# Performance work log

Hardware: AMD Instinct MI355X
Metric: run time of the kernel (lower is better)

The kernel has to match this reference:

```python
import jax, jax.numpy as jnp
import numpy as np

OUT, N_GROUPS, GROUP = 11008, 32, 128
IN = N_GROUPS * GROUP  # 4096
TOKENS = 2048


def setup_inputs() -> dict:
    key = jax.random.key(0)
    k_x, k_w, k_sc, k_s, k_b = jax.random.split(key, 5)
    x = jax.random.normal(k_x, (TOKENS, IN), dtype=jnp.float32)
    # quantized 4-bit signed weights in [-7, 7] (stored int8 in torch; int32 here)
    w_q = jax.random.randint(k_w, (OUT, N_GROUPS, GROUP), -7, 8, dtype=jnp.int32)
    # per-(out, group) positive scales, bounded away from zero like the clamp(min=1e-5)
    scales = jax.random.uniform(k_sc, (OUT, N_GROUPS, 1), dtype=jnp.float32, minval=1e-3, maxval=0.05)
    # smoothing vector: positive, bounded away from zero (it divides x)
    s = jax.random.uniform(k_s, (IN,), dtype=jnp.float32, minval=0.5, maxval=2.0)
    bias = jax.random.normal(k_b, (OUT,), dtype=jnp.float32)
    return {"x": x, "w_q": w_q, "scales": scales, "s": s, "bias": bias}


def reference(x, w_q, scales, s, bias):
    orig_dtype = x.dtype
    # group-wise dequant: [O, G, K] * [O, G, 1] -> [O, I]
    w_recon = (w_q.astype(jnp.float32) * scales).reshape(OUT, IN)
    x_f = x.astype(jnp.float32) / s  # smoothing-scale division
    y = x_f @ w_recon.T + bias
    return y.astype(orig_dtype)
```

## Files before the change

### kernel.cpp

```cpp
#include <hip/hip_runtime.h>
#include <hip/hip_bf16.h>

#define TOKENS  2048
#define IN_DIM  4096
#define OUT_DIM 11008
#define NGROUPS 32

#define BM 128
#define BN 128
#define BKB 128
#define THREADS 512
#define NKT   (IN_DIM / BKB)
#define BUFB  32768
#define BOFF  16384

using f32x4  = __attribute__((ext_vector_type(4))) float;
using i32x4  = __attribute__((ext_vector_type(4))) int;
using bf16x8 = __attribute__((ext_vector_type(8))) short;

typedef __attribute__((address_space(3))) char as3c;

static __device__ __forceinline__ short f2bf(float f) {
    union { float f; unsigned u; } v; v.f = f;
    unsigned r = v.u + 0x7FFFu + ((v.u >> 16) & 1u);
    return (short)(r >> 16);
}

static __device__ __forceinline__ int pack4(int a, int b, int c, int d) {
    return (a & 255) | ((b & 255) << 8) | ((c & 255) << 16) | ((d & 255) << 24);
}

#define SB0 __builtin_amdgcn_sched_barrier(0)
#define LDSR(dst, addr)   asm volatile("ds_read_b128 %0, %1" : "=v"(dst) : "v"(addr))
#define WAITL(n) do { asm volatile("s_waitcnt lgkmcnt(" #n ")"); SB0; } while (0)
#define WAITV(n) do { asm volatile("s_waitcnt vmcnt(" #n ")");  SB0; } while (0)

__global__ __launch_bounds__(256) void prep_a_kernel(
    const float* __restrict__ x, const float* __restrict__ s,
    char* __restrict__ Aq, float* __restrict__ sx)
{
    const int row = blockIdx.x, t = threadIdx.x;
    const float* xp = x + (size_t)row * IN_DIM + t * 16;
    const float* sp = s + t * 16;
    f32x4 v[4];
    float m = 0.f;
    #pragma unroll
    for (int q = 0; q < 4; ++q) {
        f32x4 xv = *(const f32x4*)(xp + q * 4);
        f32x4 sv = *(const f32x4*)(sp + q * 4);
        #pragma unroll
        for (int e = 0; e < 4; ++e) {
            v[q][e] = xv[e] / sv[e];
            m = fmaxf(m, fabsf(v[q][e]));
        }
    }
    #pragma unroll
    for (int off = 32; off; off >>= 1) m = fmaxf(m, __shfl_xor(m, off));
    __shared__ float wm[4];
    if ((t & 63) == 0) wm[t >> 6] = m;
    __syncthreads();
    m = fmaxf(fmaxf(wm[0], wm[1]), fmaxf(wm[2], wm[3]));
    m = fmaxf(m, 1e-20f);
    const float inv = 127.0f / m;
    i32x4 pk;
    #pragma unroll
    for (int q = 0; q < 4; ++q)
        pk[q] = pack4((int)rintf(v[q][0] * inv), (int)rintf(v[q][1] * inv),
                      (int)rintf(v[q][2] * inv), (int)rintf(v[q][3] * inv));
    ((i32x4*)(Aq + (size_t)row * IN_DIM))[t] = pk;
    if (t == 0) sx[row] = m * (1.0f / 127.0f);
}

__global__ __launch_bounds__(256) void prep_b_kernel(
    const int* __restrict__ wq, char* __restrict__ Bq)
{
    const int idx = blockIdx.x * 256 + threadIdx.x;
    const int* wp = wq + (size_t)idx * 16;
    i32x4 w0 = *(const i32x4*)wp, w1 = *(const i32x4*)(wp + 4);
    i32x4 w2 = *(const i32x4*)(wp + 8), w3 = *(const i32x4*)(wp + 12);
    i32x4 pk;
    pk[0] = pack4(w0[0], w0[1], w0[2], w0[3]);
    pk[1] = pack4(w1[0], w1[1], w1[2], w1[3]);
    pk[2] = pack4(w2[0], w2[1], w2[2], w2[3]);
    pk[3] = pack4(w3[0], w3[1], w3[2], w3[3]);
    ((i32x4*)Bq)[idx] = pk;
}

__global__ __launch_bounds__(256) void prep_sc_kernel(
    const float* __restrict__ scales, float* __restrict__ scT)
{
    const int idx = blockIdx.x * 256 + threadIdx.x;
    const int g = idx / OUT_DIM;
    const int o = idx - g * OUT_DIM;
    scT[idx] = scales[o * NGROUPS + g];
}

__global__ __launch_bounds__(THREADS, 4) void awq_gemm_i8(
    const char* __restrict__ Aq, const char* __restrict__ Bq,
    const float* __restrict__ scT, const float* __restrict__ sx,
    const float* __restrict__ bias, float* __restrict__ out)
{
    const int rb = blockIdx.x;
    const int bm = (rb >> 3) & 15;
    const int bn = (((rb >> 3) >> 4) << 3) + (rb & 7);
    if (bn >= OUT_DIM / BN) return;

    __shared__ char smem[2 * BUFB];
    as3c* ldsb = (as3c*)smem;
    const unsigned lbase = (unsigned)(size_t)ldsb;

    const int tid  = threadIdx.x;
    const int lane = tid & 63;
    const int w    = tid >> 6;
    const int wr   = w >> 2;
    const int wc   = w & 3;
    const int fr   = lane & 15;
    const int fko  = lane >> 4;

    const int h7 = fr & 7;
    const unsigned swz0 = (unsigned)(((0 * 4 + fko) ^ h7) * 16);
    const unsigned swz1 = (unsigned)(((1 * 4 + fko) ^ h7) * 16);
    const unsigned aB0 = lbase + (wr * 64 + fr) * 128 + swz0;
    const unsigned aB1 = lbase + (wr * 64 + fr) * 128 + swz1;
    const unsigned bB0 = lbase + BOFF + (wc * 32 + fr) * 128 + swz0;
    const unsigned bB1 = lbase + BOFF + (wc * 32 + fr) * 128 + swz1;

    const int srow = tid >> 3;
    const int sg   = ((tid & 7) ^ (srow & 7)) * 16;
    const char* aSrc = Aq + (size_t)(bm * BM + srow) * IN_DIM + sg;
    const char* bSrc = Bq + (size_t)(bn * BN + srow) * IN_DIM + sg;

    const float* scp = scT + bn * BN + wc * 32 + fr;

#define STG_A(Q, KT, P) __builtin_amdgcn_global_load_lds( \
    (const __attribute__((address_space(1))) void*)(const void*)(aSrc + (size_t)((Q) * 64) * IN_DIM + (KT) * BKB), \
    (__attribute__((address_space(3))) void*)(ldsb + (P) * BUFB + (Q) * 8192 + tid * 16), 16, 0, 0)
#define STG_B(Q, KT, P) __builtin_amdgcn_global_load_lds( \
    (const __attribute__((address_space(1))) void*)(const void*)(bSrc + (size_t)((Q) * 64) * IN_DIM + (KT) * BKB), \
    (__attribute__((address_space(3))) void*)(ldsb + (P) * BUFB + BOFF + (Q) * 8192 + tid * 16), 16, 0, 0)

#define SCV_GLOAD(D0, D1, G) do { \
    asm volatile("global_load_dword %0, %1, off" : "=v"(D0) : "v"(scp + (size_t)(G) * OUT_DIM)); \
    asm volatile("global_load_dword %0, %1, off" : "=v"(D1) : "v"(scp + (size_t)(G) * OUT_DIM + 16)); \
    SB0; } while (0)

    f32x4 accf[4][2];
    #pragma unroll
    for (int i = 0; i < 4; ++i) {
        accf[i][0] = (f32x4){0.f, 0.f, 0.f, 0.f};
        accf[i][1] = (f32x4){0.f, 0.f, 0.f, 0.f};
    }

    float c0, c1, n0 = 0.f, n1 = 0.f;

    STG_A(0, 0, 0); STG_A(1, 0, 0); STG_B(0, 0, 0); STG_B(1, 0, 0);
    SCV_GLOAD(c0, c1, 0);
    STG_A(0, 1, 1); STG_A(1, 1, 1); STG_B(0, 1, 1); STG_B(1, 1, 1);
    WAITV(4);
    __builtin_amdgcn_s_barrier();
    SB0;

    for (int t = 0; t < NKT; ++t) {
        const int P = t & 1;
        const unsigned po = (unsigned)(P * BUFB);
        const bool haveN = (t + 1 < NKT);
        const bool haveS = (t + 2 < NKT);

        i32x4 a[4][2], b[2][2];
        LDSR(b[0][0], bB0 + po);        LDSR(b[0][1], bB1 + po);
        LDSR(b[1][0], bB0 + po + 2048); LDSR(b[1][1], bB1 + po + 2048);
        #pragma unroll
        for (int i = 0; i < 4; ++i) {
            LDSR(a[i][0], aB0 + po + i * 2048);
            LDSR(a[i][1], aB1 + po + i * 2048);
        }
        WAITL(0);
        __builtin_amdgcn_s_barrier();
        SB0;

        if (haveN) SCV_GLOAD(n0, n1, t + 1);
        if (haveS) { STG_A(0, t + 2, P); STG_A(1, t + 2, P);
                     STG_B(0, t + 2, P); STG_B(1, t + 2, P); }

        __builtin_amdgcn_s_setprio(1);
        #pragma unroll
        for (int i = 0; i < 4; ++i) {
            i32x4 t0 = __builtin_amdgcn_mfma_i32_16x16x64_i8(a[i][0], b[0][0], (i32x4){0,0,0,0}, 0, 0, 0);
            t0       = __builtin_amdgcn_mfma_i32_16x16x64_i8(a[i][1], b[0][1], t0, 0, 0, 0);
            i32x4 t1 = __builtin_amdgcn_mfma_i32_16x16x64_i8(a[i][0], b[1][0], (i32x4){0,0,0,0}, 0, 0, 0);
            t1       = __builtin_amdgcn_mfma_i32_16x16x64_i8(a[i][1], b[1][1], t1, 0, 0, 0);
            #pragma unroll
            for (int e = 0; e < 4; ++e) {
                accf[i][0][e] += (float)t0[e] * c0;
                accf[i][1][e] += (float)t1[e] * c1;
            }
        }
        __builtin_amdgcn_s_setprio(0);

        if (t < NKT - 2) { WAITV(4); } else { WAITV(0); }
        __builtin_amdgcn_s_barrier();
        SB0;
        if (haveN) { c0 = n0; c1 = n1; }
    }

    #pragma unroll
    for (int i = 0; i < 4; ++i) {
        const int row = bm * BM + wr * 64 + i * 16 + fko * 4;
        const f32x4 sxv = *(const f32x4*)(sx + row);
        #pragma unroll
        for (int j = 0; j < 2; ++j) {
            const int col = bn * BN + wc * 32 + j * 16 + fr;
            const float bv = bias[col];
            #pragma unroll
            for (int e = 0; e < 4; ++e)
                out[(size_t)(row + e) * OUT_DIM + col] = accf[i][j][e] * sxv[e] + bv;
        }
    }

#undef STG_A
#undef STG_B
#undef SCV_GLOAD
}

__global__ __launch_bounds__(256) void awq_gemm_fb(
    const float* __restrict__ x, const int* __restrict__ wq,
    const float* __restrict__ scales, const float* __restrict__ s,
    const float* __restrict__ bias, float* __restrict__ out)
{
    __shared__ short As[128][32];
    __shared__ short Bs[128][32];
    const int tid = threadIdx.x, lane = tid & 63, wave = tid >> 6;
    const int nbn = OUT_DIM / 128;
    const int bm = blockIdx.x / nbn, bn = blockIdx.x % nbn;
    const int srow = tid >> 1, scol = (tid & 1) * 16;
    const int wm = (wave >> 1) * 64, wn = (wave & 1) * 64;
    f32x4 acc[4][4];
    #pragma unroll
    for (int i = 0; i < 4; ++i)
        #pragma unroll
        for (int j = 0; j < 4; ++j) acc[i][j] = (f32x4){0.f, 0.f, 0.f, 0.f};
    const float* xrow = x + (size_t)(bm * 128 + srow) * IN_DIM;
    const int* wrow = wq + (size_t)(bn * 128 + srow) * IN_DIM;
    const float* scrow = scales + (size_t)(bn * 128 + srow) * NGROUPS;
    const int fr = lane & 15, fk = (lane >> 4) * 8, fq = lane >> 4;
    for (int kt = 0; kt < IN_DIM / 32; ++kt) {
        const int k0 = kt * 32;
        {
            const float* xp = xrow + k0 + scol;
            const float* sp = s + k0 + scol;
            short tmp[16];
            #pragma unroll
            for (int q = 0; q < 4; ++q) {
                f32x4 xv = *(const f32x4*)(xp + q * 4);
                f32x4 sv = *(const f32x4*)(sp + q * 4);
                #pragma unroll
                for (int e = 0; e < 4; ++e) tmp[q * 4 + e] = f2bf(xv[e] / sv[e]);
            }
            #pragma unroll
            for (int e = 0; e < 16; ++e) As[srow][scol + e] = tmp[e];
        }
        {
            const float sc = scrow[kt >> 2];
            const int* wp = wrow + k0 + scol;
            short tmp[16];
            #pragma unroll
            for (int q = 0; q < 4; ++q) {
                i32x4 wv = *(const i32x4*)(wp + q * 4);
                #pragma unroll
                for (int e = 0; e < 4; ++e) tmp[q * 4 + e] = f2bf((float)wv[e] * sc);
            }
            #pragma unroll
            for (int e = 0; e < 16; ++e) Bs[srow][scol + e] = tmp[e];
        }
        __syncthreads();
        bf16x8 a[4], b[4];
        #pragma unroll
        for (int i = 0; i < 4; ++i) a[i] = *(const bf16x8*)&As[wm + i * 16 + fr][fk];
        #pragma unroll
        for (int j = 0; j < 4; ++j) b[j] = *(const bf16x8*)&Bs[wn + j * 16 + fr][fk];
        #pragma unroll
        for (int i = 0; i < 4; ++i)
            #pragma unroll
            for (int j = 0; j < 4; ++j)
                acc[i][j] = __builtin_amdgcn_mfma_f32_16x16x32_bf16(a[i], b[j], acc[i][j], 0, 0, 0);
        __syncthreads();
    }
    #pragma unroll
    for (int i = 0; i < 4; ++i) {
        const int row = bm * 128 + wm + i * 16 + fq * 4;
        #pragma unroll
        for (int j = 0; j < 4; ++j) {
            const int col = bn * 128 + wn + j * 16 + fr;
            const float bv = bias[col];
            #pragma unroll
            for (int e = 0; e < 4; ++e)
                out[(size_t)(row + e) * OUT_DIM + col] = acc[i][j][e] + bv;
        }
    }
}

extern "C" void kernel_launch(void* const* d_in, const int* in_sizes, int n_in,
                              void* d_out, int out_size, void* d_ws, size_t ws_size,
                              hipStream_t stream) {
    const float* x      = (const float*)d_in[0];
    const int*   wq     = (const int*)  d_in[1];
    const float* scales = (const float*)d_in[2];
    const float* s      = (const float*)d_in[3];
    const float* bias   = (const float*)d_in[4];
    float* out = (float*)d_out;

    const size_t off_sx = (size_t)TOKENS * IN_DIM;
    const size_t off_bq = off_sx + 8192;
    const size_t off_sc = off_bq + (size_t)OUT_DIM * IN_DIM;
    const size_t need   = off_sc + (size_t)OUT_DIM * NGROUPS * 4;

    if (ws_size >= need) {
        char*  Aq  = (char*)d_ws;
        float* sxw = (float*)((char*)d_ws + off_sx);
        char*  Bq  = (char*)d_ws + off_bq;
        float* scT = (float*)((char*)d_ws + off_sc);
        prep_a_kernel<<<TOKENS, 256, 0, stream>>>(x, s, Aq, sxw);
        prep_b_kernel<<<OUT_DIM * IN_DIM / 16 / 256, 256, 0, stream>>>(wq, Bq);
        prep_sc_kernel<<<OUT_DIM * NGROUPS / 256, 256, 0, stream>>>(scales, scT);
        awq_gemm_i8<<<1408, THREADS, 0, stream>>>(Aq, Bq, scT, sxw, bias, out);
    } else {
        awq_gemm_fb<<<(TOKENS / 128) * (OUT_DIM / 128), 256, 0, stream>>>(x, wq, scales, s, bias, out);
    }
}
```

Before: 179.6 us.

## Switch int8 GEMM to 32x32x32 MFMA with 4 waves and deferred scaling

Rewrites the main int8 GEMM to use 256 threads (4 waves, each owning a 64x64 sub-tile) with 32x32x32 int8 MFMA instructions in place of 16x16x64. LDS reads are interleaved with MFMAs through staged lgkmcnt waits. The per-group float rescale of the integer partials is deferred into the next iteration so it overlaps the next tile's MFMAs. The aim is fewer instructions and more register reuse per wave, at the cost of larger accumulator register use and lower occupancy (launch bound changed to 2 blocks per CU).

```diff
diff --git a/kernel.cpp b/kernel.cpp
--- a/kernel.cpp
+++ b/kernel.cpp
@@ -9,13 +9,14 @@
 #define BM 128
 #define BN 128
 #define BKB 128
-#define THREADS 512
+#define THREADS 256
 #define NKT   (IN_DIM / BKB)
 #define BUFB  32768
 #define BOFF  16384
 
 using f32x4  = __attribute__((ext_vector_type(4))) float;
 using i32x4  = __attribute__((ext_vector_type(4))) int;
+using i32x16 = __attribute__((ext_vector_type(16))) int;
 using bf16x8 = __attribute__((ext_vector_type(8))) short;
 
 typedef __attribute__((address_space(3))) char as3c;
@@ -31,7 +32,7 @@
 }
 
 #define SB0 __builtin_amdgcn_sched_barrier(0)
-#define LDSR(dst, addr)   asm volatile("ds_read_b128 %0, %1" : "=v"(dst) : "v"(addr))
+#define LDSRO(dst, addr, off) asm volatile("ds_read_b128 %0, %1 offset:" #off : "=v"(dst) : "v"(addr))
 #define WAITL(n) do { asm volatile("s_waitcnt lgkmcnt(" #n ")"); SB0; } while (0)
 #define WAITV(n) do { asm volatile("s_waitcnt vmcnt(" #n ")");  SB0; } while (0)
 
@@ -95,7 +96,7 @@
     scT[idx] = scales[o * NGROUPS + g];
 }
 
-__global__ __launch_bounds__(THREADS, 4) void awq_gemm_i8(
+__global__ __launch_bounds__(THREADS, 2) void awq_gemm_i8(
     const char* __restrict__ Aq, const char* __restrict__ Bq,
     const float* __restrict__ scT, const float* __restrict__ sx,
     const float* __restrict__ bias, float* __restrict__ out)
@@ -112,114 +113,160 @@
     const int tid  = threadIdx.x;
     const int lane = tid & 63;
     const int w    = tid >> 6;
-    const int wr   = w >> 2;
-    const int wc   = w & 3;
-    const int fr   = lane & 15;
-    const int fko  = lane >> 4;
-
-    const int h7 = fr & 7;
-    const unsigned swz0 = (unsigned)(((0 * 4 + fko) ^ h7) * 16);
-    const unsigned swz1 = (unsigned)(((1 * 4 + fko) ^ h7) * 16);
-    const unsigned aB0 = lbase + (wr * 64 + fr) * 128 + swz0;
-    const unsigned aB1 = lbase + (wr * 64 + fr) * 128 + swz1;
-    const unsigned bB0 = lbase + BOFF + (wc * 32 + fr) * 128 + swz0;
-    const unsigned bB1 = lbase + BOFF + (wc * 32 + fr) * 128 + swz1;
+    const int wr   = w >> 1;
+    const int wc   = w & 1;
+    const int lr   = lane & 31;
+    const int hi   = lane >> 5;
+    const int h7   = lr & 7;
+
+    const unsigned aRow = lbase + (unsigned)((wr * 64 + lr) * 128);
+    const unsigned bRow = lbase + BOFF + (unsigned)((wc * 64 + lr) * 128);
+    const unsigned aS0 = aRow + (unsigned)(((0 + hi) ^ h7) * 16);
+    const unsigned aS1 = aRow + (unsigned)(((2 + hi) ^ h7) * 16);
+    const unsigned aS2 = aRow + (unsigned)(((4 + hi) ^ h7) * 16);
+    const unsigned aS3 = aRow + (unsigned)(((6 + hi) ^ h7) * 16);
+    const unsigned bS0 = bRow + (unsigned)(((0 + hi) ^ h7) * 16);
+    const unsigned bS1 = bRow + (unsigned)(((2 + hi) ^ h7) * 16);
+    const unsigned bS2 = bRow + (unsigned)(((4 + hi) ^ h7) * 16);
+    const unsigned bS3 = bRow + (unsigned)(((6 + hi) ^ h7) * 16);
 
     const int srow = tid >> 3;
     const int sg   = ((tid & 7) ^ (srow & 7)) * 16;
     const char* aSrc = Aq + (size_t)(bm * BM + srow) * IN_DIM + sg;
     const char* bSrc = Bq + (size_t)(bn * BN + srow) * IN_DIM + sg;
 
-    const float* scp = scT + bn * BN + wc * 32 + fr;
-
-#define STG_A(Q, KT, P) __builtin_amdgcn_global_load_lds( \
-    (const __attribute__((address_space(1))) void*)(const void*)(aSrc + (size_t)((Q) * 64) * IN_DIM + (KT) * BKB), \
-    (__attribute__((address_space(3))) void*)(ldsb + (P) * BUFB + (Q) * 8192 + tid * 16), 16, 0, 0)
-#define STG_B(Q, KT, P) __builtin_amdgcn_global_load_lds( \
-    (const __attribute__((address_space(1))) void*)(const void*)(bSrc + (size_t)((Q) * 64) * IN_DIM + (KT) * BKB), \
-    (__attribute__((address_space(3))) void*)(ldsb + (P) * BUFB + BOFF + (Q) * 8192 + tid * 16), 16, 0, 0)
-
-#define SCV_GLOAD(D0, D1, G) do { \
-    asm volatile("global_load_dword %0, %1, off" : "=v"(D0) : "v"(scp + (size_t)(G) * OUT_DIM)); \
-    asm volatile("global_load_dword %0, %1, off" : "=v"(D1) : "v"(scp + (size_t)(G) * OUT_DIM + 16)); \
+    const float* scp = scT + bn * BN + wc * 64 + lr;
+
+#define STG_A(Q, SRC, P) __builtin_amdgcn_global_load_lds( \
+    (const __attribute__((address_space(1))) void*)(const void*)((SRC) + (size_t)((Q) * 32) * IN_DIM), \
+    (__attribute__((address_space(3))) void*)(ldsb + (P) * BUFB + (Q) * 4096 + tid * 16), 16, 0, 0)
+#define STG_B(Q, SRC, P) __builtin_amdgcn_global_load_lds( \
+    (const __attribute__((address_space(1))) void*)(const void*)((SRC) + (size_t)((Q) * 32) * IN_DIM), \
+    (__attribute__((address_space(3))) void*)(ldsb + (P) * BUFB + BOFF + (Q) * 4096 + tid * 16), 16, 0, 0)
+
+#define SCV(D0, D1, PTR) do { \
+    asm volatile("global_load_dword %0, %1, off" : "=v"(D0) : "v"(PTR)); \
+    asm volatile("global_load_dword %0, %1, off" : "=v"(D1) : "v"((PTR) + 32)); \
     SB0; } while (0)
 
-    f32x4 accf[4][2];
-    #pragma unroll
-    for (int i = 0; i < 4; ++i) {
-        accf[i][0] = (f32x4){0.f, 0.f, 0.f, 0.f};
-        accf[i][1] = (f32x4){0.f, 0.f, 0.f, 0.f};
-    }
-
-    float c0, c1, n0 = 0.f, n1 = 0.f;
-
-    STG_A(0, 0, 0); STG_A(1, 0, 0); STG_B(0, 0, 0); STG_B(1, 0, 0);
-    SCV_GLOAD(c0, c1, 0);
-    STG_A(0, 1, 1); STG_A(1, 1, 1); STG_B(0, 1, 1); STG_B(1, 1, 1);
-    WAITV(4);
+    float accf[2][2][16];
+    #pragma unroll
+    for (int i = 0; i < 2; ++i)
+        #pragma unroll
+        for (int j = 0; j < 2; ++j)
+            #pragma unroll
+            for (int e = 0; e < 16; ++e) accf[i][j][e] = 0.f;
+
+    i32x16 acc[2][2];
+    const i32x16 Z = {0,0,0,0,0,0,0,0,0,0,0,0,0,0,0,0};
+
+    float c0, c1, n0 = 0.f, n1 = 0.f, p0 = 0.f, p1 = 0.f;
+
+    STG_A(0, aSrc, 0); STG_A(1, aSrc, 0); STG_A(2, aSrc, 0); STG_A(3, aSrc, 0);
+    STG_B(0, bSrc, 0); STG_B(1, bSrc, 0); STG_B(2, bSrc, 0); STG_B(3, bSrc, 0);
+    SCV(c0, c1, scp);
+    STG_A(0, aSrc + BKB, 1); STG_A(1, aSrc + BKB, 1); STG_A(2, aSrc + BKB, 1); STG_A(3, aSrc + BKB, 1);
+    STG_B(0, bSrc + BKB, 1); STG_B(1, bSrc + BKB, 1); STG_B(2, bSrc + BKB, 1); STG_B(3, bSrc + BKB, 1);
+    WAITV(8);
     __builtin_amdgcn_s_barrier();
     SB0;
 
+    const char* aStg = aSrc + 2 * BKB;
+    const char* bStg = bSrc + 2 * BKB;
+    const float* scN = scp + OUT_DIM;
+
     for (int t = 0; t < NKT; ++t) {
-        const int P = t & 1;
-        const unsigned po = (unsigned)(P * BUFB);
-        const bool haveN = (t + 1 < NKT);
-        const bool haveS = (t + 2 < NKT);
-
-        i32x4 a[4][2], b[2][2];
-        LDSR(b[0][0], bB0 + po);        LDSR(b[0][1], bB1 + po);
-        LDSR(b[1][0], bB0 + po + 2048); LDSR(b[1][1], bB1 + po + 2048);
-        #pragma unroll
-        for (int i = 0; i < 4; ++i) {
-            LDSR(a[i][0], aB0 + po + i * 2048);
-            LDSR(a[i][1], aB1 + po + i * 2048);
-        }
+        const unsigned po = (unsigned)((t & 1) * BUFB);
+        i32x4 a[2][4], b[2][4];
+        const unsigned pa0 = aS0 + po, pa1 = aS1 + po, pa2 = aS2 + po, pa3 = aS3 + po;
+        const unsigned pb0 = bS0 + po, pb1 = bS1 + po, pb2 = bS2 + po, pb3 = bS3 + po;
+        LDSRO(a[0][0], pa0, 0); LDSRO(a[1][0], pa0, 4096);
+        LDSRO(b[0][0], pb0, 0); LDSRO(b[1][0], pb0, 4096);
+        LDSRO(a[0][1], pa1, 0); LDSRO(a[1][1], pa1, 4096);
+        LDSRO(b[0][1], pb1, 0); LDSRO(b[1][1], pb1, 4096);
+        LDSRO(a[0][2], pa2, 0); LDSRO(a[1][2], pa2, 4096);
+        LDSRO(b[0][2], pb2, 0); LDSRO(b[1][2], pb2, 4096);
+        LDSRO(a[0][3], pa3, 0); LDSRO(a[1][3], pa3, 4096);
+        LDSRO(b[0][3], pb3, 0); LDSRO(b[1][3], pb3, 4096);
+
+        if (t > 0) {
+            #pragma unroll
+            for (int i = 0; i < 2; ++i)
+                #pragma unroll
+                for (int e = 0; e < 16; ++e) {
+                    accf[i][0][e] += (float)acc[i][0][e] * p0;
+                    accf[i][1][e] += (float)acc[i][1][e] * p1;
+                }
+        }
+
+        __builtin_amdgcn_s_setprio(1);
+        WAITL(12);
+        acc[0][0] = __builtin_amdgcn_mfma_i32_32x32x32_i8(a[0][0], b[0][0], Z, 0, 0, 0);
+        acc[0][1] = __builtin_amdgcn_mfma_i32_32x32x32_i8(a[0][0], b[1][0], Z, 0, 0, 0);
+        acc[1][0] = __builtin_amdgcn_mfma_i32_32x32x32_i8(a[1][0], b[0][0], Z, 0, 0, 0);
+        acc[1][1] = __builtin_amdgcn_mfma_i32_32x32x32_i8(a[1][0], b[1][0], Z, 0, 0, 0);
+        WAITL(8);
+        acc[0][0] = __builtin_amdgcn_mfma_i32_32x32x32_i8(a[0][1], b[0][1], acc[0][0], 0, 0, 0);
+        acc[0][1] = __builtin_amdgcn_mfma_i32_32x32x32_i8(a[0][1], b[1][1], acc[0][1], 0, 0, 0);
+        acc[1][0] = __builtin_amdgcn_mfma_i32_32x32x32_i8(a[1][1], b[0][1], acc[1][0], 0, 0, 0);
+        acc[1][1] = __builtin_amdgcn_mfma_i32_32x32x32_i8(a[1][1], b[1][1], acc[1][1], 0, 0, 0);
+        WAITL(4);
+        acc[0][0] = __builtin_amdgcn_mfma_i32_32x32x32_i8(a[0][2], b[0][2], acc[0][0], 0, 0, 0);
+        acc[0][1] = __builtin_amdgcn_mfma_i32_32x32x32_i8(a[0][2], b[1][2], acc[0][1], 0, 0, 0);
+        acc[1][0] = __builtin_amdgcn_mfma_i32_32x32x32_i8(a[1][2], b[0][2], acc[1][0], 0, 0, 0);
+        acc[1][1] = __builtin_amdgcn_mfma_i32_32x32x32_i8(a[1][2], b[1][2], acc[1][1], 0, 0, 0);
         WAITL(0);
         __builtin_amdgcn_s_barrier();
         SB0;
-
-        if (haveN) SCV_GLOAD(n0, n1, t + 1);
-        if (haveS) { STG_A(0, t + 2, P); STG_A(1, t + 2, P);
-                     STG_B(0, t + 2, P); STG_B(1, t + 2, P); }
-
-        __builtin_amdgcn_s_setprio(1);
-        #pragma unroll
-        for (int i = 0; i < 4; ++i) {
-            i32x4 t0 = __builtin_amdgcn_mfma_i32_16x16x64_i8(a[i][0], b[0][0], (i32x4){0,0,0,0}, 0, 0, 0);
-            t0       = __builtin_amdgcn_mfma_i32_16x16x64_i8(a[i][1], b[0][1], t0, 0, 0, 0);
-            i32x4 t1 = __builtin_amdgcn_mfma_i32_16x16x64_i8(a[i][0], b[1][0], (i32x4){0,0,0,0}, 0, 0, 0);
-            t1       = __builtin_amdgcn_mfma_i32_16x16x64_i8(a[i][1], b[1][1], t1, 0, 0, 0);
-            #pragma unroll
-            for (int e = 0; e < 4; ++e) {
-                accf[i][0][e] += (float)t0[e] * c0;
-                accf[i][1][e] += (float)t1[e] * c1;
-            }
-        }
+        acc[0][0] = __builtin_amdgcn_mfma_i32_32x32x32_i8(a[0][3], b[0][3], acc[0][0], 0, 0, 0);
+        acc[0][1] = __builtin_amdgcn_mfma_i32_32x32x32_i8(a[0][3], b[1][3], acc[0][1], 0, 0, 0);
+        acc[1][0] = __builtin_amdgcn_mfma_i32_32x32x32_i8(a[1][3], b[0][3], acc[1][0], 0, 0, 0);
+        acc[1][1] = __builtin_amdgcn_mfma_i32_32x32x32_i8(a[1][3], b[1][3], acc[1][1], 0, 0, 0);
         __builtin_amdgcn_s_setprio(0);
 
-        if (t < NKT - 2) { WAITV(4); } else { WAITV(0); }
+        const bool haveN = (t + 1 < NKT);
+        if (haveN) SCV(n0, n1, scN);
+        if (t + 2 < NKT) {
+            STG_A(0, aStg, (t & 1)); STG_A(1, aStg, (t & 1)); STG_A(2, aStg, (t & 1)); STG_A(3, aStg, (t & 1));
+            STG_B(0, bStg, (t & 1)); STG_B(1, bStg, (t & 1)); STG_B(2, bStg, (t & 1)); STG_B(3, bStg, (t & 1));
+        }
+        aStg += BKB; bStg += BKB; scN += OUT_DIM;
+
+        if (t < NKT - 2) { WAITV(8); } else { WAITV(0); }
         __builtin_amdgcn_s_barrier();
         SB0;
+        p0 = c0; p1 = c1;
         if (haveN) { c0 = n0; c1 = n1; }
     }
 
     #pragma unroll
-    for (int i = 0; i < 4; ++i) {
-        const int row = bm * BM + wr * 64 + i * 16 + fko * 4;
-        const f32x4 sxv = *(const f32x4*)(sx + row);
-        #pragma unroll
-        for (int j = 0; j < 2; ++j) {
-            const int col = bn * BN + wc * 32 + j * 16 + fr;
-            const float bv = bias[col];
-            #pragma unroll
-            for (int e = 0; e < 4; ++e)
-                out[(size_t)(row + e) * OUT_DIM + col] = accf[i][j][e] * sxv[e] + bv;
+    for (int i = 0; i < 2; ++i)
+        #pragma unroll
+        for (int e = 0; e < 16; ++e) {
+            accf[i][0][e] += (float)acc[i][0][e] * p0;
+            accf[i][1][e] += (float)acc[i][1][e] * p1;
+        }
+
+    const int colBase = bn * BN + wc * 64 + lr;
+    const float bv0 = bias[colBase];
+    const float bv1 = bias[colBase + 32];
+    #pragma unroll
+    for (int i = 0; i < 2; ++i) {
+        #pragma unroll
+        for (int q = 0; q < 4; ++q) {
+            const int r0 = bm * BM + wr * 64 + i * 32 + q * 8 + hi * 4;
+            const f32x4 sxv = *(const f32x4*)(sx + r0);
+            #pragma unroll
+            for (int e = 0; e < 4; ++e) {
+                out[(size_t)(r0 + e) * OUT_DIM + colBase]      = accf[i][0][q * 4 + e] * sxv[e] + bv0;
+                out[(size_t)(r0 + e) * OUT_DIM + colBase + 32] = accf[i][1][q * 4 + e] * sxv[e] + bv1;
+            }
         }
     }
 
 #undef STG_A
 #undef STG_B
-#undef SCV_GLOAD
+#undef SCV
 }
 
 __global__ __launch_bounds__(256) void awq_gemm_fb(
```

Measured after the change: 229.9 us. +28.0%, slower.

## Load weight fragments straight to registers and software-pipeline the k-loop

Applied to the files above, without the earlier changes.

Weight (B) tiles no longer go through LDS. Each wave loads its int8 MFMA fragments directly from global memory into registers, one k-step ahead, alongside the per-group scales. That halves the LDS footprint to just the activation buffers. The k-loop is unrolled by two, with fixed ping-pong buffers and immediate-offset ds_reads interleaved with the MFMAs, and the next activation stage is issued mid-iteration. This cuts LDS traffic and barrier-bound stalls, but waves that share columns now fetch the same B data twice from global/L2, and register pressure rises.

```diff
diff --git a/kernel.cpp b/kernel.cpp
--- a/kernel.cpp
+++ b/kernel.cpp
@@ -11,8 +11,7 @@
 #define BKB 128
 #define THREADS 512
 #define NKT   (IN_DIM / BKB)
-#define BUFB  32768
-#define BOFF  16384
+#define BUFB  16384
 
 using f32x4  = __attribute__((ext_vector_type(4))) float;
 using i32x4  = __attribute__((ext_vector_type(4))) int;
@@ -31,7 +30,7 @@
 }
 
 #define SB0 __builtin_amdgcn_sched_barrier(0)
-#define LDSR(dst, addr)   asm volatile("ds_read_b128 %0, %1" : "=v"(dst) : "v"(addr))
+#define LDSRO(dst, addr, off) asm volatile("ds_read_b128 %0, %1 offset:" #off : "=v"(dst) : "v"(addr))
 #define WAITL(n) do { asm volatile("s_waitcnt lgkmcnt(" #n ")"); SB0; } while (0)
 #define WAITV(n) do { asm volatile("s_waitcnt vmcnt(" #n ")");  SB0; } while (0)
 
@@ -122,27 +121,42 @@
     const unsigned swz1 = (unsigned)(((1 * 4 + fko) ^ h7) * 16);
     const unsigned aB0 = lbase + (wr * 64 + fr) * 128 + swz0;
     const unsigned aB1 = lbase + (wr * 64 + fr) * 128 + swz1;
-    const unsigned bB0 = lbase + BOFF + (wc * 32 + fr) * 128 + swz0;
-    const unsigned bB1 = lbase + BOFF + (wc * 32 + fr) * 128 + swz1;
 
     const int srow = tid >> 3;
     const int sg   = ((tid & 7) ^ (srow & 7)) * 16;
     const char* aSrc = Aq + (size_t)(bm * BM + srow) * IN_DIM + sg;
-    const char* bSrc = Bq + (size_t)(bn * BN + srow) * IN_DIM + sg;
 
     const float* scp = scT + bn * BN + wc * 32 + fr;
 
-#define STG_A(Q, KT, P) __builtin_amdgcn_global_load_lds( \
-    (const __attribute__((address_space(1))) void*)(const void*)(aSrc + (size_t)((Q) * 64) * IN_DIM + (KT) * BKB), \
+    const char* bfp0 = Bq + (size_t)(bn * BN + wc * 32 + fr) * IN_DIM + fko * 16;
+    const char* bfp1 = bfp0 + (size_t)16 * IN_DIM;
+
+#define STG_A(Q, OFFB, P) __builtin_amdgcn_global_load_lds( \
+    (const __attribute__((address_space(1))) void*)(const void*)(aStg + (OFFB) + (size_t)((Q) * 64) * IN_DIM), \
     (__attribute__((address_space(3))) void*)(ldsb + (P) * BUFB + (Q) * 8192 + tid * 16), 16, 0, 0)
-#define STG_B(Q, KT, P) __builtin_amdgcn_global_load_lds( \
-    (const __attribute__((address_space(1))) void*)(const void*)(bSrc + (size_t)((Q) * 64) * IN_DIM + (KT) * BKB), \
-    (__attribute__((address_space(3))) void*)(ldsb + (P) * BUFB + BOFF + (Q) * 8192 + tid * 16), 16, 0, 0)
-
-#define SCV_GLOAD(D0, D1, G) do { \
-    asm volatile("global_load_dword %0, %1, off" : "=v"(D0) : "v"(scp + (size_t)(G) * OUT_DIM)); \
-    asm volatile("global_load_dword %0, %1, off" : "=v"(D1) : "v"(scp + (size_t)(G) * OUT_DIM + 16)); \
+
+#define BFRAG4(D00, D01, D10, D11, O0, O1) do { \
+    asm volatile("global_load_dwordx4 %0, %1, off offset:" #O0 : "=v"(D00) : "v"(bfp0)); \
+    asm volatile("global_load_dwordx4 %0, %1, off offset:" #O1 : "=v"(D01) : "v"(bfp0)); \
+    asm volatile("global_load_dwordx4 %0, %1, off offset:" #O0 : "=v"(D10) : "v"(bfp1)); \
+    asm volatile("global_load_dwordx4 %0, %1, off offset:" #O1 : "=v"(D11) : "v"(bfp1)); \
     SB0; } while (0)
+
+#define SCV(D0, D1, PTR) do { \
+    asm volatile("global_load_dword %0, %1, off" : "=v"(D0) : "v"(PTR)); \
+    asm volatile("global_load_dword %0, %1, off" : "=v"(D1) : "v"((PTR) + 16)); \
+    SB0; } while (0)
+
+#define MMI(A0, A1, B00, B01, B10, B11, F0, F1) do { \
+    i32x4 t0 = __builtin_amdgcn_mfma_i32_16x16x64_i8(A0, B00, (i32x4){0,0,0,0}, 0, 0, 0); \
+    t0       = __builtin_amdgcn_mfma_i32_16x16x64_i8(A1, B01, t0, 0, 0, 0); \
+    i32x4 t1 = __builtin_amdgcn_mfma_i32_16x16x64_i8(A0, B10, (i32x4){0,0,0,0}, 0, 0, 0); \
+    t1       = __builtin_amdgcn_mfma_i32_16x16x64_i8(A1, B11, t1, 0, 0, 0); \
+    _Pragma("unroll") \
+    for (int e = 0; e < 4; ++e) { \
+        F0[e] += (float)t0[e] * c0; \
+        F1[e] += (float)t1[e] * c1; \
+    } } while (0)
 
     f32x4 accf[4][2];
     #pragma unroll
@@ -151,56 +165,78 @@
         accf[i][1] = (f32x4){0.f, 0.f, 0.f, 0.f};
     }
 
+    i32x4 b0_00, b0_01, b0_10, b0_11;
+    i32x4 b1_00, b1_01, b1_10, b1_11;
     float c0, c1, n0 = 0.f, n1 = 0.f;
 
-    STG_A(0, 0, 0); STG_A(1, 0, 0); STG_B(0, 0, 0); STG_B(1, 0, 0);
-    SCV_GLOAD(c0, c1, 0);
-    STG_A(0, 1, 1); STG_A(1, 1, 1); STG_B(0, 1, 1); STG_B(1, 1, 1);
-    WAITV(4);
+    const char*  aStg = aSrc;
+    const float* scN  = scp + OUT_DIM;
+
+    STG_A(0, 0, 0); STG_A(1, 0, 0);
+    SB0;
+    BFRAG4(b0_00, b0_01, b0_10, b0_11, 0, 64);
+    SCV(c0, c1, scp);
+    STG_A(0, 128, 1); STG_A(1, 128, 1);
+    SB0;
+    WAITV(2);
     __builtin_amdgcn_s_barrier();
     SB0;
 
-    for (int t = 0; t < NKT; ++t) {
-        const int P = t & 1;
-        const unsigned po = (unsigned)(P * BUFB);
-        const bool haveN = (t + 1 < NKT);
-        const bool haveS = (t + 2 < NKT);
-
-        i32x4 a[4][2], b[2][2];
-        LDSR(b[0][0], bB0 + po);        LDSR(b[0][1], bB1 + po);
-        LDSR(b[1][0], bB0 + po + 2048); LDSR(b[1][1], bB1 + po + 2048);
-        #pragma unroll
-        for (int i = 0; i < 4; ++i) {
-            LDSR(a[i][0], aB0 + po + i * 2048);
-            LDSR(a[i][1], aB1 + po + i * 2048);
-        }
+    for (int it = 0; it < NKT / 2; ++it) {
+        const bool last = (it == NKT / 2 - 1);
+        i32x4 a00, a01, a10, a11, a20, a21, a30, a31;
+
+        LDSRO(a00, aB0, 0);    LDSRO(a01, aB1, 0);
+        LDSRO(a10, aB0, 2048); LDSRO(a11, aB1, 2048);
+        BFRAG4(b1_00, b1_01, b1_10, b1_11, 128, 192);
+        SCV(n0, n1, scN);
+        __builtin_amdgcn_s_setprio(1);
+        WAITL(2);
+        LDSRO(a20, aB0, 4096); LDSRO(a21, aB1, 4096);
+        MMI(a00, a01, b0_00, b0_01, b0_10, b0_11, accf[0][0], accf[0][1]);
+        WAITL(2);
+        LDSRO(a30, aB0, 6144); LDSRO(a31, aB1, 6144);
+        MMI(a10, a11, b0_00, b0_01, b0_10, b0_11, accf[1][0], accf[1][1]);
+        WAITL(2);
+        MMI(a20, a21, b0_00, b0_01, b0_10, b0_11, accf[2][0], accf[2][1]);
         WAITL(0);
         __builtin_amdgcn_s_barrier();
         SB0;
-
-        if (haveN) SCV_GLOAD(n0, n1, t + 1);
-        if (haveS) { STG_A(0, t + 2, P); STG_A(1, t + 2, P);
-                     STG_B(0, t + 2, P); STG_B(1, t + 2, P); }
-
+        if (!last) { STG_A(0, 256, 0); STG_A(1, 256, 0); }
+        SB0;
+        MMI(a30, a31, b0_00, b0_01, b0_10, b0_11, accf[3][0], accf[3][1]);
+        __builtin_amdgcn_s_setprio(0);
+        if (!last) { WAITV(2); } else { WAITV(0); }
+        __builtin_amdgcn_s_barrier();
+        SB0;
+        c0 = n0; c1 = n1;
+
+        LDSRO(a00, aB0, 16384); LDSRO(a01, aB1, 16384);
+        LDSRO(a10, aB0, 18432); LDSRO(a11, aB1, 18432);
+        if (!last) { BFRAG4(b0_00, b0_01, b0_10, b0_11, 256, 320); SCV(n0, n1, scN + OUT_DIM); }
         __builtin_amdgcn_s_setprio(1);
-        #pragma unroll
-        for (int i = 0; i < 4; ++i) {
-            i32x4 t0 = __builtin_amdgcn_mfma_i32_16x16x64_i8(a[i][0], b[0][0], (i32x4){0,0,0,0}, 0, 0, 0);
-            t0       = __builtin_amdgcn_mfma_i32_16x16x64_i8(a[i][1], b[0][1], t0, 0, 0, 0);
-            i32x4 t1 = __builtin_amdgcn_mfma_i32_16x16x64_i8(a[i][0], b[1][0], (i32x4){0,0,0,0}, 0, 0, 0);
-            t1       = __builtin_amdgcn_mfma_i32_16x16x64_i8(a[i][1], b[1][1], t1, 0, 0, 0);
-            #pragma unroll
-            for (int e = 0; e < 4; ++e) {
-                accf[i][0][e] += (float)t0[e] * c0;
-                accf[i][1][e] += (float)t1[e] * c1;
-            }
-        }
+        WAITL(2);
+        LDSRO(a20, aB0, 20480); LDSRO(a21, aB1, 20480);
+        MMI(a00, a01, b1_00, b1_01, b1_10, b1_11, accf[0][0], accf[0][1]);
+        WAITL(2);
+        LDSRO(a30, aB0, 22528); LDSRO(a31, aB1, 22528);
+        MMI(a10, a11, b1_00, b1_01, b1_10, b1_11, accf[1][0], accf[1][1]);
+        WAITL(2);
+        MMI(a20, a21, b1_00, b1_01, b1_10, b1_11, accf[2][0], accf[2][1]);
+        WAITL(0);
+        __builtin_amdgcn_s_barrier();
+        SB0;
+        if (!last) { STG_A(0, 384, 1); STG_A(1, 384, 1); }
+        SB0;
+        MMI(a30, a31, b1_00, b1_01, b1_10, b1_11, accf[3][0], accf[3][1]);
         __builtin_amdgcn_s_setprio(0);
-
-        if (t < NKT - 2) { WAITV(4); } else { WAITV(0); }
+        if (!last) { WAITV(2); } else { WAITV(0); }
         __builtin_amdgcn_s_barrier();
         SB0;
-        if (haveN) { c0 = n0; c1 = n1; }
+        if (!last) { c0 = n0; c1 = n1; }
+
+        aStg += 256; scN += 2 * OUT_DIM;
+        bfp0 += 256; bfp1 += 256;
     }
 
     #pragma unroll
@@ -218,8 +254,9 @@
     }
 
 #undef STG_A
-#undef STG_B
-#undef SCV_GLOAD
+#undef BFRAG4
+#undef SCV
+#undef MMI
 }
 
 __global__ __launch_bounds__(256) void awq_gemm_fb(
```

Result: slower. 409.6 us (+128.1%).

## Widen int8 GEMM tile to 128x256 with BK=64 and a two-step unrolled pipeline

Applied to the files above, without the earlier changes.

Changes the int8 MFMA GEMM block tile from 128x128 with K-step 128 to 128x256 with K-step 64, so each wave now covers 64x64 outputs. The main loop is unrolled over the two LDS buffers, so LDS reads use fixed immediate offsets, and each group scale is loaded once per 128-wide group. The aim is more reuse of each staged A tile and fewer blocks (768 instead of 1408) loading overlapping data. In exchange it uses more accumulator registers, lowers the launch-bounds occupancy hint from 4 to 2, and makes the swizzle and the wait counts more intricate.

```diff
diff --git a/kernel.cpp b/kernel.cpp
--- a/kernel.cpp
+++ b/kernel.cpp
@@ -7,12 +7,13 @@
 #define NGROUPS 32
 
 #define BM 128
-#define BN 128
-#define BKB 128
+#define BN 256
+#define BK 64
 #define THREADS 512
-#define NKT   (IN_DIM / BKB)
-#define BUFB  32768
-#define BOFF  16384
+#define NT    (IN_DIM / BK)
+#define ABYTES (BM * BK)
+#define BBYTES (BN * BK)
+#define BUFB  (ABYTES + BBYTES)
 
 using f32x4  = __attribute__((ext_vector_type(4))) float;
 using i32x4  = __attribute__((ext_vector_type(4))) int;
@@ -31,7 +32,7 @@
 }
 
 #define SB0 __builtin_amdgcn_sched_barrier(0)
-#define LDSR(dst, addr)   asm volatile("ds_read_b128 %0, %1" : "=v"(dst) : "v"(addr))
+#define LDSRO(dst, addr, off) asm volatile("ds_read_b128 %0, %1 offset:" #off : "=v"(dst) : "v"(addr))
 #define WAITL(n) do { asm volatile("s_waitcnt lgkmcnt(" #n ")"); SB0; } while (0)
 #define WAITV(n) do { asm volatile("s_waitcnt vmcnt(" #n ")");  SB0; } while (0)
 
@@ -95,7 +96,7 @@
     scT[idx] = scales[o * NGROUPS + g];
 }
 
-__global__ __launch_bounds__(THREADS, 4) void awq_gemm_i8(
+__global__ __launch_bounds__(THREADS, 2) void awq_gemm_i8(
     const char* __restrict__ Aq, const char* __restrict__ Bq,
     const float* __restrict__ scT, const float* __restrict__ sx,
     const float* __restrict__ bias, float* __restrict__ out)
@@ -117,90 +118,110 @@
     const int fr   = lane & 15;
     const int fko  = lane >> 4;
 
-    const int h7 = fr & 7;
-    const unsigned swz0 = (unsigned)(((0 * 4 + fko) ^ h7) * 16);
-    const unsigned swz1 = (unsigned)(((1 * 4 + fko) ^ h7) * 16);
-    const unsigned aB0 = lbase + (wr * 64 + fr) * 128 + swz0;
-    const unsigned aB1 = lbase + (wr * 64 + fr) * 128 + swz1;
-    const unsigned bB0 = lbase + BOFF + (wc * 32 + fr) * 128 + swz0;
-    const unsigned bB1 = lbase + BOFF + (wc * 32 + fr) * 128 + swz1;
-
-    const int srow = tid >> 3;
-    const int sg   = ((tid & 7) ^ (srow & 7)) * 16;
-    const char* aSrc = Aq + (size_t)(bm * BM + srow) * IN_DIM + sg;
-    const char* bSrc = Bq + (size_t)(bn * BN + srow) * IN_DIM + sg;
-
-    const float* scp = scT + bn * BN + wc * 32 + fr;
-
-#define STG_A(Q, KT, P) __builtin_amdgcn_global_load_lds( \
-    (const __attribute__((address_space(1))) void*)(const void*)(aSrc + (size_t)((Q) * 64) * IN_DIM + (KT) * BKB), \
-    (__attribute__((address_space(3))) void*)(ldsb + (P) * BUFB + (Q) * 8192 + tid * 16), 16, 0, 0)
-#define STG_B(Q, KT, P) __builtin_amdgcn_global_load_lds( \
-    (const __attribute__((address_space(1))) void*)(const void*)(bSrc + (size_t)((Q) * 64) * IN_DIM + (KT) * BKB), \
-    (__attribute__((address_space(3))) void*)(ldsb + (P) * BUFB + BOFF + (Q) * 8192 + tid * 16), 16, 0, 0)
-
-#define SCV_GLOAD(D0, D1, G) do { \
-    asm volatile("global_load_dword %0, %1, off" : "=v"(D0) : "v"(scp + (size_t)(G) * OUT_DIM)); \
-    asm volatile("global_load_dword %0, %1, off" : "=v"(D1) : "v"(scp + (size_t)(G) * OUT_DIM + 16)); \
+    const unsigned sw4  = (unsigned)((fko ^ (fr & 3)) * 16);
+    const unsigned aAddr = lbase + (unsigned)((wr * 64 + fr) * 64) + sw4;
+    const unsigned bAddr = lbase + ABYTES + (unsigned)((wc * 64 + fr) * 64) + sw4;
+
+    const int sr = tid >> 2;
+    const int sg = ((tid & 3) ^ (sr & 3)) * 16;
+    const char* aSrc  = Aq + (size_t)(bm * BM + sr) * IN_DIM + sg;
+    const char* bSrc  = Bq + (size_t)(bn * BN + sr) * IN_DIM + sg;
+    const char* bSrc2 = bSrc + (size_t)128 * IN_DIM;
+
+    const float* scp = scT + bn * BN + wc * 64 + fr;
+
+#define STG(PA, PB, PB2, P) do { \
+    __builtin_amdgcn_global_load_lds((const __attribute__((address_space(1))) void*)(const void*)(PA), \
+        (__attribute__((address_space(3))) void*)(ldsb + (P) * BUFB + tid * 16), 16, 0, 0); \
+    __builtin_amdgcn_global_load_lds((const __attribute__((address_space(1))) void*)(const void*)(PB), \
+        (__attribute__((address_space(3))) void*)(ldsb + (P) * BUFB + ABYTES + tid * 16), 16, 0, 0); \
+    __builtin_amdgcn_global_load_lds((const __attribute__((address_space(1))) void*)(const void*)(PB2), \
+        (__attribute__((address_space(3))) void*)(ldsb + (P) * BUFB + ABYTES + 8192 + tid * 16), 16, 0, 0); \
     SB0; } while (0)
 
-    f32x4 accf[4][2];
-    #pragma unroll
-    for (int i = 0; i < 4; ++i) {
-        accf[i][0] = (f32x4){0.f, 0.f, 0.f, 0.f};
-        accf[i][1] = (f32x4){0.f, 0.f, 0.f, 0.f};
-    }
-
-    float c0, c1, n0 = 0.f, n1 = 0.f;
-
-    STG_A(0, 0, 0); STG_A(1, 0, 0); STG_B(0, 0, 0); STG_B(1, 0, 0);
-    SCV_GLOAD(c0, c1, 0);
-    STG_A(0, 1, 1); STG_A(1, 1, 1); STG_B(0, 1, 1); STG_B(1, 1, 1);
-    WAITV(4);
+#define SCV4(D0, D1, D2, D3, PTR) do { \
+    asm volatile("global_load_dword %0, %1, off"            : "=v"(D0) : "v"(PTR)); \
+    asm volatile("global_load_dword %0, %1, off offset:64"  : "=v"(D1) : "v"(PTR)); \
+    asm volatile("global_load_dword %0, %1, off offset:128" : "=v"(D2) : "v"(PTR)); \
+    asm volatile("global_load_dword %0, %1, off offset:192" : "=v"(D3) : "v"(PTR)); \
+    SB0; } while (0)
+
+#define QUADJ(J, CJ) do { \
+    i32x4 t0 = __builtin_amdgcn_mfma_i32_16x16x64_i8(a[0], b[J], (i32x4){0,0,0,0}, 0, 0, 0); \
+    i32x4 t1 = __builtin_amdgcn_mfma_i32_16x16x64_i8(a[1], b[J], (i32x4){0,0,0,0}, 0, 0, 0); \
+    i32x4 t2 = __builtin_amdgcn_mfma_i32_16x16x64_i8(a[2], b[J], (i32x4){0,0,0,0}, 0, 0, 0); \
+    i32x4 t3 = __builtin_amdgcn_mfma_i32_16x16x64_i8(a[3], b[J], (i32x4){0,0,0,0}, 0, 0, 0); \
+    _Pragma("unroll") \
+    for (int e = 0; e < 4; ++e) { \
+        accf[0][J][e] += (float)t0[e] * (CJ); \
+        accf[1][J][e] += (float)t1[e] * (CJ); \
+        accf[2][J][e] += (float)t2[e] * (CJ); \
+        accf[3][J][e] += (float)t3[e] * (CJ); \
+    } } while (0)
+
+#define COMPUTE() do { \
+    __builtin_amdgcn_s_setprio(1); \
+    QUADJ(0, c0); QUADJ(1, c1); QUADJ(2, c2); QUADJ(3, c3); \
+    __builtin_amdgcn_s_setprio(0); } while (0)
+
+    f32x4 accf[4][4];
+    #pragma unroll
+    for (int i = 0; i < 4; ++i)
+        #pragma unroll
+        for (int j = 0; j < 4; ++j) accf[i][j] = (f32x4){0.f, 0.f, 0.f, 0.f};
+
+    i32x4 a[4], b[4];
+    float c0, c1, c2, c3, n0 = 0.f, n1 = 0.f, n2 = 0.f, n3 = 0.f;
+
+    STG(aSrc, bSrc, bSrc2, 0);
+    SCV4(c0, c1, c2, c3, scp);
+    STG(aSrc + BK, bSrc + BK, bSrc2 + BK, 1);
+    WAITV(3);
     __builtin_amdgcn_s_barrier();
     SB0;
 
-    for (int t = 0; t < NKT; ++t) {
-        const int P = t & 1;
-        const unsigned po = (unsigned)(P * BUFB);
-        const bool haveN = (t + 1 < NKT);
-        const bool haveS = (t + 2 < NKT);
-
-        i32x4 a[4][2], b[2][2];
-        LDSR(b[0][0], bB0 + po);        LDSR(b[0][1], bB1 + po);
-        LDSR(b[1][0], bB0 + po + 2048); LDSR(b[1][1], bB1 + po + 2048);
-        #pragma unroll
-        for (int i = 0; i < 4; ++i) {
-            LDSR(a[i][0], aB0 + po + i * 2048);
-            LDSR(a[i][1], aB1 + po + i * 2048);
-        }
+    const char*  aStg  = aSrc  + 2 * BK;
+    const char*  bStg  = bSrc  + 2 * BK;
+    const char*  bStg2 = bSrc2 + 2 * BK;
+    const float* scN   = scp + OUT_DIM;
+
+    for (int p = 0; p < NT / 2; ++p) {
+        const bool haveN = (p < NT / 2 - 1);
+
+        LDSRO(a[0], aAddr, 0);    LDSRO(a[1], aAddr, 1024);
+        LDSRO(a[2], aAddr, 2048); LDSRO(a[3], aAddr, 3072);
+        LDSRO(b[0], bAddr, 0);    LDSRO(b[1], bAddr, 1024);
+        LDSRO(b[2], bAddr, 2048); LDSRO(b[3], bAddr, 3072);
         WAITL(0);
         __builtin_amdgcn_s_barrier();
         SB0;
-
-        if (haveN) SCV_GLOAD(n0, n1, t + 1);
-        if (haveS) { STG_A(0, t + 2, P); STG_A(1, t + 2, P);
-                     STG_B(0, t + 2, P); STG_B(1, t + 2, P); }
-
-        __builtin_amdgcn_s_setprio(1);
-        #pragma unroll
-        for (int i = 0; i < 4; ++i) {
-            i32x4 t0 = __builtin_amdgcn_mfma_i32_16x16x64_i8(a[i][0], b[0][0], (i32x4){0,0,0,0}, 0, 0, 0);
-            t0       = __builtin_amdgcn_mfma_i32_16x16x64_i8(a[i][1], b[0][1], t0, 0, 0, 0);
-            i32x4 t1 = __builtin_amdgcn_mfma_i32_16x16x64_i8(a[i][0], b[1][0], (i32x4){0,0,0,0}, 0, 0, 0);
-            t1       = __builtin_amdgcn_mfma_i32_16x16x64_i8(a[i][1], b[1][1], t1, 0, 0, 0);
-            #pragma unroll
-            for (int e = 0; e < 4; ++e) {
-                accf[i][0][e] += (float)t0[e] * c0;
-                accf[i][1][e] += (float)t1[e] * c1;
-            }
-        }
-        __builtin_amdgcn_s_setprio(0);
-
-        if (t < NKT - 2) { WAITV(4); } else { WAITV(0); }
+        if (haveN) STG(aStg, bStg, bStg2, 0);
+        SB0;
+        COMPUTE();
+        if (haveN) { WAITV(3); } else { WAITV(0); }
         __builtin_amdgcn_s_barrier();
         SB0;
-        if (haveN) { c0 = n0; c1 = n1; }
+
+        LDSRO(a[0], aAddr, 24576); LDSRO(a[1], aAddr, 25600);
+        LDSRO(a[2], aAddr, 26624); LDSRO(a[3], aAddr, 27648);
+        LDSRO(b[0], bAddr, 24576); LDSRO(b[1], bAddr, 25600);
+        LDSRO(b[2], bAddr, 26624); LDSRO(b[3], bAddr, 27648);
+        WAITL(0);
+        __builtin_amdgcn_s_barrier();
+        SB0;
+        if (haveN) {
+            SCV4(n0, n1, n2, n3, scN);
+            STG(aStg + BK, bStg + BK, bStg2 + BK, 1);
+        }
+        SB0;
+        COMPUTE();
+        if (haveN) { WAITV(3); } else { WAITV(0); }
+        __builtin_amdgcn_s_barrier();
+        SB0;
+        if (haveN) {
+            c0 = n0; c1 = n1; c2 = n2; c3 = n3;
+            aStg += 2 * BK; bStg += 2 * BK; bStg2 += 2 * BK; scN += OUT_DIM;
+        }
     }
 
     #pragma unroll
@@ -208,8 +229,8 @@
         const int row = bm * BM + wr * 64 + i * 16 + fko * 4;
         const f32x4 sxv = *(const f32x4*)(sx + row);
         #pragma unroll
-        for (int j = 0; j < 2; ++j) {
-            const int col = bn * BN + wc * 32 + j * 16 + fr;
+        for (int j = 0; j < 4; ++j) {
+            const int col = bn * BN + wc * 64 + j * 16 + fr;
             const float bv = bias[col];
             #pragma unroll
             for (int e = 0; e < 4; ++e)
@@ -217,9 +238,10 @@
         }
     }
 
-#undef STG_A
-#undef STG_B
-#undef SCV_GLOAD
+#undef STG
+#undef SCV4
+#undef QUADJ
+#undef COMPUTE
 }
 
 __global__ __launch_bounds__(256) void awq_gemm_fb(
@@ -322,7 +344,7 @@
         prep_a_kernel<<<TOKENS, 256, 0, stream>>>(x, s, Aq, sxw);
         prep_b_kernel<<<OUT_DIM * IN_DIM / 16 / 256, 256, 0, stream>>>(wq, Bq);
         prep_sc_kernel<<<OUT_DIM * NGROUPS / 256, 256, 0, stream>>>(scales, scT);
-        awq_gemm_i8<<<1408, THREADS, 0, stream>>>(Aq, Bq, scT, sxw, bias, out);
+        awq_gemm_i8<<<768, THREADS, 0, stream>>>(Aq, Bq, scT, sxw, bias, out);
     } else {
         awq_gemm_fb<<<(TOKENS / 128) * (OUT_DIM / 128), 256, 0, stream>>>(x, wq, scales, s, bias, out);
     }
```

After: 265.2 us. 47.7% more time.
